# Kernel tuning notes

Hardware: AMD Instinct MI355X
Metric: run time of the kernel (lower is better)

## Reference

```python
import jax, jax.numpy as jnp
from jax import lax
import numpy as np

P = 2          # cost exponent: C(x,y) = |x-y|^p / p
BLUR = 0.05    # final epsilon = BLUR**P
SCALING = 0.5  # geomloss epsilon-scaling factor


def _cost(x, y):
    # squared Euclidean distance / 2  (geomloss p=2 cost), shape [N, M]
    sq = jnp.sum(x * x, axis=1)[:, None] + jnp.sum(y * y, axis=1)[None, :] - 2.0 * (x @ y.T)
    return jnp.maximum(sq, 0.0) * 0.5


def _softmin(eps, C, h):
    # h: log-weights (+ potential/eps) over columns of C; returns [rows]
    return -eps * jax.nn.logsumexp(h[None, :] - C / eps, axis=1)


def setup_inputs() -> dict:
    key = jax.random.key(0)
    k1, k2 = jax.random.split(key)
    N, M, D = 8192, 8192, 64
    g = jax.random.normal(k1, (N, D), jnp.float32)
    Y = jax.random.normal(k2, (M, D), jnp.float32) + 1.0  # shifted target measure
    # geomloss epsilon_schedule: diameter**p annealed by SCALING**p down to BLUR**p
    xy = np.concatenate([np.asarray(g), np.asarray(Y)], axis=0)
    diameter = float(np.linalg.norm(xy.max(0) - xy.min(0)))
    eps_list = ([diameter ** P]
                + [float(np.exp(e)) for e in np.arange(P * np.log(diameter), P * np.log(BLUR), P * np.log(SCALING))]
                + [BLUR ** P])
    return {"g": g, "Y": Y, "eps_list": jnp.asarray(eps_list, jnp.float32)}


def reference(g, Y, eps_list):
    x, y = g, Y
    N, M = x.shape[0], y.shape[0]
    a_log = jnp.full((N,), -jnp.log(jnp.float32(N)), x.dtype)  # uniform log-weights
    b_log = jnp.full((M,), -jnp.log(jnp.float32(M)), y.dtype)

    C_xy, C_yx = _cost(x, y), _cost(y, x)
    C_xx, C_yy = _cost(x, x), _cost(y, y)
    # Sinkhorn loop runs on detached costs (geomloss runs it under no_grad)
    sg = lax.stop_gradient
    Cxy_s, Cyx_s, Cxx_s, Cyy_s = sg(C_xy), sg(C_yx), sg(C_xx), sg(C_yy)

    eps0 = eps_list[0]
    f_aa = _softmin(eps0, Cxx_s, a_log)
    g_bb = _softmin(eps0, Cyy_s, b_log)
    g_ab = _softmin(eps0, Cyx_s, a_log)
    f_ba = _softmin(eps0, Cxy_s, b_log)

    def step(carry, eps):
        f_aa, g_bb, g_ab, f_ba = carry
        ft = _softmin(eps, Cxy_s, b_log + g_ab / eps)
        gt = _softmin(eps, Cyx_s, a_log + f_ba / eps)
        ftaa = _softmin(eps, Cxx_s, a_log + f_aa / eps)
        gtbb = _softmin(eps, Cyy_s, b_log + g_bb / eps)
        # symmetrized (averaged) dual updates, as in geomloss
        return (0.5 * (f_aa + ftaa), 0.5 * (g_bb + gtbb),
                0.5 * (g_ab + gt), 0.5 * (f_ba + ft)), None

    (f_aa, g_bb, g_ab, f_ba), _ = lax.scan(step, (f_aa, g_bb, g_ab, f_ba), eps_list)

    # last extrapolation at eps = blur**p: differentiable costs, detached potentials
    eps = eps_list[-1]
    f_ba_f = _softmin(eps, C_xy, sg(b_log + g_ab / eps))
    g_ab_f = _softmin(eps, C_yx, sg(a_log + f_ba / eps))
    f_aa_f = _softmin(eps, C_xx, sg(a_log + f_aa / eps))
    g_bb_f = _softmin(eps, C_yy, sg(b_log + g_bb / eps))

    # S_eps(alpha, beta) = <alpha, f_ba - f_aa> + <beta, g_ab - g_bb> (uniform weights)
    return jnp.mean(f_ba_f - f_aa_f) + jnp.mean(g_ab_f - g_bb_f)
```

## Files before the change

kernel.cpp:

```cpp
#include <hip/hip_runtime.h>
#include <math.h>

#define D 64
#define BR 128
#define NCHUNK 8
#define YLD 72
#define LOG2E 1.4426950408889634f
#define LN2   0.6931471805599453f

typedef __attribute__((ext_vector_type(8))) __bf16 bf16x8;
typedef __attribute__((ext_vector_type(4))) float  floatx4;
typedef __attribute__((ext_vector_type(2))) float  floatx2;

static __device__ __forceinline__ float exp2fast(float x) {
#if __has_builtin(__builtin_amdgcn_exp2f)
    return __builtin_amdgcn_exp2f(x);
#else
    return exp2f(x);
#endif
}
static __device__ __forceinline__ float log2fast(float x) {
#if __has_builtin(__builtin_amdgcn_logf)
    return __builtin_amdgcn_logf(x);
#else
    return log2f(x);
#endif
}
static __device__ __forceinline__ float max3f(float a, float b, float c) {
    return fmaxf(fmaxf(a, b), c);
}

static __device__ __forceinline__ unsigned short f2bf_rne(float f) {
    unsigned u = __float_as_uint(f);
    return (unsigned short)((u + 0x7fffu + ((u >> 16) & 1u)) >> 16);
}

struct OpDesc {
    const unsigned short* xh;
    const unsigned short* yh;
    const float* cc;
    const float* sqn_col;
    float* pm; float* ps;
    int n_rows, n_cols, symmetric, pad;
};
struct P4 { OpDesc op[4]; };

struct MDesc {
    const float* pm; const float* ps;
    const float* sqn_row;
    const float* oldpot;
    float* newpot;
    float* ccout;
    float wlog_c;
    int n_rows, mix, pad;
};
struct M4 { MDesc op[4]; };

__global__ void cvt_kernel(const float* __restrict__ x,
                           unsigned short* __restrict__ xh, int n_elem8)
{
    int i = blockIdx.x * blockDim.x + threadIdx.x;
    if (i >= n_elem8) return;
    const float4* xp = (const float4*)x;
    float4 v0 = xp[i * 2], v1 = xp[i * 2 + 1];
    float v[8] = {v0.x, v0.y, v0.z, v0.w, v1.x, v1.y, v1.z, v1.w};
    unsigned h[8];
#pragma unroll
    for (int k = 0; k < 8; ++k) h[k] = f2bf_rne(v[k]);
    uint4 ph;
    ph.x = h[0] | (h[1] << 16); ph.y = h[2] | (h[3] << 16);
    ph.z = h[4] | (h[5] << 16); ph.w = h[6] | (h[7] << 16);
    ((uint4*)xh)[i] = ph;
}

__global__ void sqnorm_kernel(const float* __restrict__ x, float* __restrict__ sqn, int n)
{
    int i = blockIdx.x * blockDim.x + threadIdx.x;
    if (i >= n) return;
    const float4* xp = (const float4*)(x + (size_t)i * D);
    float sum = 0.0f;
#pragma unroll
    for (int k = 0; k < D / 4; ++k) {
        float4 v = xp[k];
        sum += v.x * v.x + v.y * v.y + v.z * v.z + v.w * v.w;
    }
    sqn[i] = 0.5f * sum;
}

__global__ void init_cc_kernel(const float* __restrict__ sqn_x, const float* __restrict__ sqn_y,
                               float* cc0, float* cc1, float* cc2, float* cc3,
                               const float* __restrict__ eps_list,
                               float a_log, float b_log, int N, int M)
{
    int i = blockIdx.x * blockDim.x + threadIdx.x;
    float inv_e0 = 1.0f / eps_list[0];
    if (i < M) { float v = (b_log - sqn_y[i] * inv_e0) * LOG2E; cc0[i] = v; cc3[i] = v; }
    if (i < N) { float v = (a_log - sqn_x[i] * inv_e0) * LOG2E; cc1[i] = v; cc2[i] = v; }
}

__global__ __launch_bounds__(256)
void softmin_mfma4(P4 p4, const float* __restrict__ eps_list, int eps_idx)
{
    __shared__ __bf16 yth[128 * YLD];

    const OpDesc o = p4.op[blockIdx.z];
    const int t    = threadIdx.x;
    const int lane = t & 63;
    const int w    = t >> 6;
    const int lx   = lane & 15;
    const int q    = lane >> 4;
    const int row0 = blockIdx.x * BR;
    const int chunk = blockIdx.y;
    const int cols_per_chunk = o.n_cols / NCHUNK;
    const int nsub = cols_per_chunk / 128;

    const float eps     = eps_list[eps_idx];
    const float inv_eps = 1.0f / eps;
    const float scale2  = inv_eps * LOG2E;
    const floatx2 s2v   = (floatx2){scale2, scale2};
    const floatx4 Z4    = (floatx4){0.f, 0.f, 0.f, 0.f};

    bf16x8 ah[2][2];
    {
        const int r0 = row0 + w * 32;
#pragma unroll
        for (int rt = 0; rt < 2; ++rt)
#pragma unroll
            for (int ks = 0; ks < 2; ++ks)
                ah[rt][ks] = *(const bf16x8*)(o.xh + (size_t)(r0 + rt * 16 + lx) * D + ks * 32 + q * 8);
    }

    const int diag_blk = o.symmetric && ((row0 / cols_per_chunk) == chunk);
    float sqr[8];
    if (diag_blk) {
#pragma unroll
        for (int idx = 0; idx < 8; ++idx) {
            int row = row0 + w * 32 + (idx >> 2) * 16 + q * 4 + (idx & 3);
            sqr[idx] = o.sqn_col[row];
        }
    }

    float m[8], s[8];
#pragma unroll
    for (int i = 0; i < 8; ++i) { m[i] = -__builtin_inff(); s[i] = 0.0f; }

    for (int sub = 0; sub < nsub; ++sub) {
        const int col0 = chunk * cols_per_chunk + sub * 128;

        __syncthreads();
        {
            const uint4* gh = (const uint4*)(o.yh + (size_t)col0 * D);
#pragma unroll
            for (int i = 0; i < 4; ++i) {
                int c = t + i * 256;
                int row = c >> 3, part = c & 7;
                uint4 vh = gh[c];
                *(uint4*)(&yth[row * YLD + part * 8]) = vh;
            }
        }
        __syncthreads();

        float cc[8];
#pragma unroll
        for (int ct = 0; ct < 8; ++ct) cc[ct] = o.cc[col0 + ct * 16 + lx];

        floatx4 acc[8][2];
#pragma unroll
        for (int ct = 0; ct < 8; ++ct) {
            const int cl = ct * 16 + lx;
            bf16x8 bh0 = *(const bf16x8*)&yth[cl * YLD + q * 8];
            bf16x8 bh1 = *(const bf16x8*)&yth[cl * YLD + 32 + q * 8];
#pragma unroll
            for (int rt = 0; rt < 2; ++rt) {
                floatx4 a = __builtin_amdgcn_mfma_f32_16x16x32_bf16(ah[rt][0], bh0, Z4, 0, 0, 0);
                acc[ct][rt] = __builtin_amdgcn_mfma_f32_16x16x32_bf16(ah[rt][1], bh1, a, 0, 0, 0);
            }
        }

        if (diag_blk && col0 == row0) {
#pragma unroll
            for (int rt = 0; rt < 2; ++rt)
#pragma unroll
                for (int r = 0; r < 4; ++r) {
                    if (lx == q * 4 + r) {
                        const float v = 2.0f * sqr[rt * 4 + r];
#pragma unroll
                        for (int ct = 0; ct < 8; ++ct)
                            if (ct == w * 2 + rt) acc[ct][rt][r] = v;
                    }
                }
        }

        floatx2 ccv[4];
#pragma unroll
        for (int cp = 0; cp < 4; ++cp)
            ccv[cp] = (floatx2){cc[cp * 2], cc[cp * 2 + 1]};

#pragma unroll
        for (int rt = 0; rt < 2; ++rt)
#pragma unroll
            for (int r = 0; r < 4; ++r) {
                const int idx = rt * 4 + r;
                floatx2 zv[4];
#pragma unroll
                for (int cp = 0; cp < 4; ++cp) {
                    floatx2 av = (floatx2){acc[cp * 2][rt][r], acc[cp * 2 + 1][rt][r]};
                    zv[cp] = __builtin_elementwise_fma(av, s2v, ccv[cp]);
                }
                float M = max3f(zv[0].x, zv[0].y, zv[1].x);
                M = max3f(M, zv[1].y, zv[2].x);
                M = max3f(M, zv[2].y, zv[3].x);
                M = max3f(M, zv[3].y, m[idx]);
                const floatx2 Mv = (floatx2){M, M};
                floatx2 sv = (floatx2){0.f, 0.f};
#pragma unroll
                for (int cp = 0; cp < 4; ++cp) {
                    floatx2 dd = zv[cp] - Mv;
                    sv += (floatx2){exp2fast(dd.x), exp2fast(dd.y)};
                }
                s[idx] = fmaf(s[idx], exp2fast(m[idx] - M), sv.x + sv.y);
                m[idx] = M;
            }
    }

#pragma unroll
    for (int idx = 0; idx < 8; ++idx) {
        float mm = m[idx], ss = s[idx];
#pragma unroll
        for (int d = 1; d < 16; d <<= 1) {
            float mo = __shfl_xor(mm, d, 64);
            float so = __shfl_xor(ss, d, 64);
            float M = fmaxf(mm, mo);
            ss = ss * exp2fast(mm - M) + so * exp2fast(mo - M);
            mm = M;
        }
        if (lx == 0) {
            const int rt = idx >> 2, r = idx & 3;
            const int row = row0 + w * 32 + rt * 16 + q * 4 + r;
            o.pm[chunk * o.n_rows + row] = mm;
            o.ps[chunk * o.n_rows + row] = ss;
        }
    }
}

__global__ void softmin_merge4(M4 m4, const float* __restrict__ eps_list,
                               int eps_idx, int eps_idx_next)
{
    const MDesc o = m4.op[blockIdx.y];
    int i = blockIdx.x * blockDim.x + threadIdx.x;
    if (i >= o.n_rows) return;
    const float eps = eps_list[eps_idx];
    float M = -__builtin_inff();
    for (int c = 0; c < NCHUNK; ++c) M = fmaxf(M, o.pm[c * o.n_rows + i]);
    float S = 0.0f;
    for (int c = 0; c < NCHUNK; ++c) S += o.ps[c * o.n_rows + i] * exp2fast(o.pm[c * o.n_rows + i] - M);
    const float sq = o.sqn_row[i];
    float val = sq - eps * LN2 * (M + log2fast(S));
    float nv = o.mix ? 0.5f * (o.oldpot[i] + val) : val;
    o.newpot[i] = nv;
    if (o.ccout) {
        float inv_en = 1.0f / eps_list[eps_idx_next];
        o.ccout[i] = (o.wlog_c + (nv - sq) * inv_en) * LOG2E;
    }
}

__global__ void final_reduce(const float* __restrict__ f_ba_f, const float* __restrict__ f_aa_f,
                             const float* __restrict__ g_ab_f, const float* __restrict__ g_bb_f,
                             int n, int mcount, float* __restrict__ out)
{
    __shared__ float red[256];
    float s1 = 0.0f, s2 = 0.0f;
    for (int i = threadIdx.x; i < n; i += 256)      s1 += (f_ba_f[i] - f_aa_f[i]);
    for (int i = threadIdx.x; i < mcount; i += 256) s2 += (g_ab_f[i] - g_bb_f[i]);
    red[threadIdx.x] = s1 / (float)n + s2 / (float)mcount;
    __syncthreads();
    for (int off = 128; off > 0; off >>= 1) {
        if (threadIdx.x < off) red[threadIdx.x] += red[threadIdx.x + off];
        __syncthreads();
    }
    if (threadIdx.x == 0) out[0] = red[0];
}

extern "C" void kernel_launch(void* const* d_in, const int* in_sizes, int n_in,
                              void* d_out, int out_size, void* d_ws, size_t ws_size,
                              hipStream_t stream)
{
    const float* g        = (const float*)d_in[0];
    const float* Y        = (const float*)d_in[1];
    const float* eps_list = (const float*)d_in[2];
    const int N = in_sizes[0] / D;
    const int M = in_sizes[1] / D;
    const int L = in_sizes[2];
    const float a_log = -logf((float)N);
    const float b_log = -logf((float)M);
    const int NM = (N > M) ? N : M;
    const size_t PMS = (size_t)NCHUNK * NM;

    unsigned short* us = (unsigned short*)d_ws;
    unsigned short* gxh = us; us += (size_t)N * D;
    unsigned short* gyh = us; us += (size_t)M * D;

    float* ws = (float*)us;
    float* sqn_x = ws; ws += N;
    float* sqn_y = ws; ws += M;
    float* fba[2]; fba[0] = ws; ws += N; fba[1] = ws; ws += N;
    float* gab[2]; gab[0] = ws; ws += M; gab[1] = ws; ws += M;
    float* fa[2];  fa[0]  = ws; ws += N; fa[1]  = ws; ws += N;
    float* gb[2];  gb[0]  = ws; ws += M; gb[1]  = ws; ws += M;
    float* f_ba_f = ws; ws += N;
    float* g_ab_f = ws; ws += M;
    float* f_aa_f = ws; ws += N;
    float* g_bb_f = ws; ws += M;
    float* cc[2][4];
    for (int pbuf = 0; pbuf < 2; ++pbuf)
        for (int i = 0; i < 4; ++i) { cc[pbuf][i] = ws; ws += NM; }
    float* pm = ws; ws += 4 * PMS;
    float* psb = ws; ws += 4 * PMS;

    sqnorm_kernel<<<(N + 255) / 256, 256, 0, stream>>>(g, sqn_x, N);
    sqnorm_kernel<<<(M + 255) / 256, 256, 0, stream>>>(Y, sqn_y, M);
    cvt_kernel<<<(N * D / 8 + 255) / 256, 256, 0, stream>>>(g, gxh, N * D / 8);
    cvt_kernel<<<(M * D / 8 + 255) / 256, 256, 0, stream>>>(Y, gyh, M * D / 8);
    init_cc_kernel<<<(NM + 255) / 256, 256, 0, stream>>>(sqn_x, sqn_y,
        cc[0][0], cc[0][1], cc[0][2], cc[0][3], eps_list, a_log, b_log, N, M);

    auto phase = [&](int eidx, int eidx_next, int mix, int cur, int ccp, int writecc,
                     float* out0, float* out1, float* out2, float* out3) {
        P4 p;
        p.op[0] = { gxh, gyh, cc[ccp][0], sqn_y, pm + 0 * PMS, psb + 0 * PMS, N, M, 0, 0 };
        p.op[1] = { gyh, gxh, cc[ccp][1], sqn_x, pm + 1 * PMS, psb + 1 * PMS, M, N, 0, 0 };
        p.op[2] = { gxh, gxh, cc[ccp][2], sqn_x, pm + 2 * PMS, psb + 2 * PMS, N, N, 1, 0 };
        p.op[3] = { gyh, gyh, cc[ccp][3], sqn_y, pm + 3 * PMS, psb + 3 * PMS, M, M, 1, 0 };
        softmin_mfma4<<<dim3(NM / BR, NCHUNK, 4), 256, 0, stream>>>(p, eps_list, eidx);

        M4 mm;
        mm.op[0] = { pm + 0 * PMS, psb + 0 * PMS, sqn_x, fba[cur], out0,
                     writecc ? cc[ccp ^ 1][1] : nullptr, a_log, N, mix, 0 };
        mm.op[1] = { pm + 1 * PMS, psb + 1 * PMS, sqn_y, gab[cur], out1,
                     writecc ? cc[ccp ^ 1][0] : nullptr, b_log, M, mix, 0 };
        mm.op[2] = { pm + 2 * PMS, psb + 2 * PMS, sqn_x, fa[cur], out2,
                     writecc ? cc[ccp ^ 1][2] : nullptr, a_log, N, mix, 0 };
        mm.op[3] = { pm + 3 * PMS, psb + 3 * PMS, sqn_y, gb[cur], out3,
                     writecc ? cc[ccp ^ 1][3] : nullptr, b_log, M, mix, 0 };
        softmin_merge4<<<dim3((NM + 255) / 256, 4), 256, 0, stream>>>(mm, eps_list, eidx, eidx_next);
    };

    phase(0, 0, 0, 0, 0, 1, fba[0], gab[0], fa[0], gb[0]);
    int cur = 0, ccp = 1;

    for (int k = 0; k < L; ++k) {
        int en = (k + 1 < L) ? (k + 1) : (L - 1);
        phase(k, en, 1, cur, ccp, 1, fba[cur ^ 1], gab[cur ^ 1], fa[cur ^ 1], gb[cur ^ 1]);
        cur ^= 1; ccp ^= 1;
    }

    phase(L - 1, L - 1, 0, cur, ccp, 0, f_ba_f, g_ab_f, f_aa_f, g_bb_f);

    final_reduce<<<1, 256, 0, stream>>>(f_ba_f, f_aa_f, g_ab_f, g_bb_f, N, M, (float*)d_out);
}
```

Before: 1.251 ms.

## Convert softmin kernel to persistent blocks with atomic work-queue scheduling

The softmin MFMA kernel now launches a fixed grid of 768 persistent blocks that pull (op, row-block, chunk) work units from a global atomic counter instead of using a 3D grid. The counter is reset by init_cc and by each merge kernel so the next phase starts fresh. This is meant to improve load balance and cut block launch and tail overhead across the 2048 work units. It adds an atomic plus two barriers per unit, and the A-fragment and state setup now runs inside the unit loop.

```diff
diff --git a/kernel.cpp b/kernel.cpp
--- a/kernel.cpp
+++ b/kernel.cpp
@@ -5,6 +5,7 @@
 #define BR 128
 #define NCHUNK 8
 #define YLD 72
+#define NPERS 768
 #define LOG2E 1.4426950408889634f
 #define LN2   0.6931471805599453f
 
@@ -90,29 +91,28 @@
 __global__ void init_cc_kernel(const float* __restrict__ sqn_x, const float* __restrict__ sqn_y,
                                float* cc0, float* cc1, float* cc2, float* cc3,
                                const float* __restrict__ eps_list,
-                               float a_log, float b_log, int N, int M)
+                               float a_log, float b_log, int N, int M,
+                               int* __restrict__ counter)
 {
     int i = blockIdx.x * blockDim.x + threadIdx.x;
+    if (i == 0) counter[0] = 0;
     float inv_e0 = 1.0f / eps_list[0];
     if (i < M) { float v = (b_log - sqn_y[i] * inv_e0) * LOG2E; cc0[i] = v; cc3[i] = v; }
     if (i < N) { float v = (a_log - sqn_x[i] * inv_e0) * LOG2E; cc1[i] = v; cc2[i] = v; }
 }
 
 __global__ __launch_bounds__(256)
-void softmin_mfma4(P4 p4, const float* __restrict__ eps_list, int eps_idx)
+void softmin_mfma4(P4 p4, const float* __restrict__ eps_list, int eps_idx,
+                   int* __restrict__ counter, int rbmax, int nunits)
 {
     __shared__ __bf16 yth[128 * YLD];
-
-    const OpDesc o = p4.op[blockIdx.z];
+    __shared__ int u_sh;
+
     const int t    = threadIdx.x;
     const int lane = t & 63;
     const int w    = t >> 6;
     const int lx   = lane & 15;
     const int q    = lane >> 4;
-    const int row0 = blockIdx.x * BR;
-    const int chunk = blockIdx.y;
-    const int cols_per_chunk = o.n_cols / NCHUNK;
-    const int nsub = cols_per_chunk / 128;
 
     const float eps     = eps_list[eps_idx];
     const float inv_eps = 1.0f / eps;
@@ -120,132 +120,152 @@
     const floatx2 s2v   = (floatx2){scale2, scale2};
     const floatx4 Z4    = (floatx4){0.f, 0.f, 0.f, 0.f};
 
-    bf16x8 ah[2][2];
-    {
-        const int r0 = row0 + w * 32;
-#pragma unroll
-        for (int rt = 0; rt < 2; ++rt)
-#pragma unroll
-            for (int ks = 0; ks < 2; ++ks)
-                ah[rt][ks] = *(const bf16x8*)(o.xh + (size_t)(r0 + rt * 16 + lx) * D + ks * 32 + q * 8);
-    }
-
-    const int diag_blk = o.symmetric && ((row0 / cols_per_chunk) == chunk);
-    float sqr[8];
-    if (diag_blk) {
-#pragma unroll
-        for (int idx = 0; idx < 8; ++idx) {
-            int row = row0 + w * 32 + (idx >> 2) * 16 + q * 4 + (idx & 3);
-            sqr[idx] = o.sqn_col[row];
+    for (;;) {
+        __syncthreads();
+        if (t == 0) u_sh = atomicAdd(counter, 1);
+        __syncthreads();
+        const int u = u_sh;
+        if (u >= nunits) break;
+
+        const int op    = u / (rbmax * NCHUNK);
+        const int rem   = u - op * (rbmax * NCHUNK);
+        const int rb    = rem >> 3;
+        const int chunk = rem & (NCHUNK - 1);
+        const OpDesc o  = p4.op[op];
+        const int row0  = rb * BR;
+        if (row0 >= o.n_rows) continue;
+        const int cols_per_chunk = o.n_cols / NCHUNK;
+        const int nsub = cols_per_chunk / 128;
+
+        bf16x8 ah[2][2];
+        {
+            const int r0 = row0 + w * 32;
+#pragma unroll
+            for (int rt = 0; rt < 2; ++rt)
+#pragma unroll
+                for (int ks = 0; ks < 2; ++ks)
+                    ah[rt][ks] = *(const bf16x8*)(o.xh + (size_t)(r0 + rt * 16 + lx) * D + ks * 32 + q * 8);
         }
-    }
-
-    float m[8], s[8];
-#pragma unroll
-    for (int i = 0; i < 8; ++i) { m[i] = -__builtin_inff(); s[i] = 0.0f; }
-
-    for (int sub = 0; sub < nsub; ++sub) {
-        const int col0 = chunk * cols_per_chunk + sub * 128;
-
-        __syncthreads();
-        {
-            const uint4* gh = (const uint4*)(o.yh + (size_t)col0 * D);
-#pragma unroll
-            for (int i = 0; i < 4; ++i) {
-                int c = t + i * 256;
-                int row = c >> 3, part = c & 7;
-                uint4 vh = gh[c];
-                *(uint4*)(&yth[row * YLD + part * 8]) = vh;
+
+        const int diag_blk = o.symmetric && ((row0 / cols_per_chunk) == chunk);
+        float sqr[8];
+        if (diag_blk) {
+#pragma unroll
+            for (int idx = 0; idx < 8; ++idx) {
+                int row = row0 + w * 32 + (idx >> 2) * 16 + q * 4 + (idx & 3);
+                sqr[idx] = o.sqn_col[row];
             }
         }
-        __syncthreads();
-
-        float cc[8];
-#pragma unroll
-        for (int ct = 0; ct < 8; ++ct) cc[ct] = o.cc[col0 + ct * 16 + lx];
-
-        floatx4 acc[8][2];
-#pragma unroll
-        for (int ct = 0; ct < 8; ++ct) {
-            const int cl = ct * 16 + lx;
-            bf16x8 bh0 = *(const bf16x8*)&yth[cl * YLD + q * 8];
-            bf16x8 bh1 = *(const bf16x8*)&yth[cl * YLD + 32 + q * 8];
-#pragma unroll
-            for (int rt = 0; rt < 2; ++rt) {
-                floatx4 a = __builtin_amdgcn_mfma_f32_16x16x32_bf16(ah[rt][0], bh0, Z4, 0, 0, 0);
-                acc[ct][rt] = __builtin_amdgcn_mfma_f32_16x16x32_bf16(ah[rt][1], bh1, a, 0, 0, 0);
-            }
-        }
-
-        if (diag_blk && col0 == row0) {
+
+        float m[8], s[8];
+#pragma unroll
+        for (int i = 0; i < 8; ++i) { m[i] = -__builtin_inff(); s[i] = 0.0f; }
+
+        for (int sub = 0; sub < nsub; ++sub) {
+            const int col0 = chunk * cols_per_chunk + sub * 128;
+
+            __syncthreads();
+            {
+                const uint4* gh = (const uint4*)(o.yh + (size_t)col0 * D);
+#pragma unroll
+                for (int i = 0; i < 4; ++i) {
+                    int c = t + i * 256;
+                    int row = c >> 3, part = c & 7;
+                    uint4 vh = gh[c];
+                    *(uint4*)(&yth[row * YLD + part * 8]) = vh;
+                }
+            }
+            __syncthreads();
+
+            float cc[8];
+#pragma unroll
+            for (int ct = 0; ct < 8; ++ct) cc[ct] = o.cc[col0 + ct * 16 + lx];
+
+            floatx4 acc[8][2];
+#pragma unroll
+            for (int ct = 0; ct < 8; ++ct) {
+                const int cl = ct * 16 + lx;
+                bf16x8 bh0 = *(const bf16x8*)&yth[cl * YLD + q * 8];
+                bf16x8 bh1 = *(const bf16x8*)&yth[cl * YLD + 32 + q * 8];
+#pragma unroll
+                for (int rt = 0; rt < 2; ++rt) {
+                    floatx4 a = __builtin_amdgcn_mfma_f32_16x16x32_bf16(ah[rt][0], bh0, Z4, 0, 0, 0);
+                    acc[ct][rt] = __builtin_amdgcn_mfma_f32_16x16x32_bf16(ah[rt][1], bh1, a, 0, 0, 0);
+                }
+            }
+
+            if (diag_blk && col0 == row0) {
+#pragma unroll
+                for (int rt = 0; rt < 2; ++rt)
+#pragma unroll
+                    for (int r = 0; r < 4; ++r) {
+                        if (lx == q * 4 + r) {
+                            const float v = 2.0f * sqr[rt * 4 + r];
+#pragma unroll
+                            for (int ct = 0; ct < 8; ++ct)
+                                if (ct == w * 2 + rt) acc[ct][rt][r] = v;
+                        }
+                    }
+            }
+
+            floatx2 ccv[4];
+#pragma unroll
+            for (int cp = 0; cp < 4; ++cp)
+                ccv[cp] = (floatx2){cc[cp * 2], cc[cp * 2 + 1]};
+
 #pragma unroll
             for (int rt = 0; rt < 2; ++rt)
 #pragma unroll
                 for (int r = 0; r < 4; ++r) {
-                    if (lx == q * 4 + r) {
-                        const float v = 2.0f * sqr[rt * 4 + r];
-#pragma unroll
-                        for (int ct = 0; ct < 8; ++ct)
-                            if (ct == w * 2 + rt) acc[ct][rt][r] = v;
+                    const int idx = rt * 4 + r;
+                    floatx2 zv[4];
+#pragma unroll
+                    for (int cp = 0; cp < 4; ++cp) {
+                        floatx2 av = (floatx2){acc[cp * 2][rt][r], acc[cp * 2 + 1][rt][r]};
+                        zv[cp] = __builtin_elementwise_fma(av, s2v, ccv[cp]);
                     }
+                    float M = max3f(zv[0].x, zv[0].y, zv[1].x);
+                    M = max3f(M, zv[1].y, zv[2].x);
+                    M = max3f(M, zv[2].y, zv[3].x);
+                    M = max3f(M, zv[3].y, m[idx]);
+                    const floatx2 Mv = (floatx2){M, M};
+                    floatx2 sv = (floatx2){0.f, 0.f};
+#pragma unroll
+                    for (int cp = 0; cp < 4; ++cp) {
+                        floatx2 dd = zv[cp] - Mv;
+                        sv += (floatx2){exp2fast(dd.x), exp2fast(dd.y)};
+                    }
+                    s[idx] = fmaf(s[idx], exp2fast(m[idx] - M), sv.x + sv.y);
+                    m[idx] = M;
                 }
         }
 
-        floatx2 ccv[4];
-#pragma unroll
-        for (int cp = 0; cp < 4; ++cp)
-            ccv[cp] = (floatx2){cc[cp * 2], cc[cp * 2 + 1]};
-
-#pragma unroll
-        for (int rt = 0; rt < 2; ++rt)
-#pragma unroll
-            for (int r = 0; r < 4; ++r) {
-                const int idx = rt * 4 + r;
-                floatx2 zv[4];
-#pragma unroll
-                for (int cp = 0; cp < 4; ++cp) {
-                    floatx2 av = (floatx2){acc[cp * 2][rt][r], acc[cp * 2 + 1][rt][r]};
-                    zv[cp] = __builtin_elementwise_fma(av, s2v, ccv[cp]);
-                }
-                float M = max3f(zv[0].x, zv[0].y, zv[1].x);
-                M = max3f(M, zv[1].y, zv[2].x);
-                M = max3f(M, zv[2].y, zv[3].x);
-                M = max3f(M, zv[3].y, m[idx]);
-                const floatx2 Mv = (floatx2){M, M};
-                floatx2 sv = (floatx2){0.f, 0.f};
-#pragma unroll
-                for (int cp = 0; cp < 4; ++cp) {
-                    floatx2 dd = zv[cp] - Mv;
-                    sv += (floatx2){exp2fast(dd.x), exp2fast(dd.y)};
-                }
-                s[idx] = fmaf(s[idx], exp2fast(m[idx] - M), sv.x + sv.y);
-                m[idx] = M;
-            }
-    }
-
-#pragma unroll
-    for (int idx = 0; idx < 8; ++idx) {
-        float mm = m[idx], ss = s[idx];
-#pragma unroll
-        for (int d = 1; d < 16; d <<= 1) {
-            float mo = __shfl_xor(mm, d, 64);
-            float so = __shfl_xor(ss, d, 64);
-            float M = fmaxf(mm, mo);
-            ss = ss * exp2fast(mm - M) + so * exp2fast(mo - M);
-            mm = M;
+#pragma unroll
+        for (int idx = 0; idx < 8; ++idx) {
+            float mm = m[idx], ss = s[idx];
+#pragma unroll
+            for (int d = 1; d < 16; d <<= 1) {
+                float mo = __shfl_xor(mm, d, 64);
+                float so = __shfl_xor(ss, d, 64);
+                float M = fmaxf(mm, mo);
+                ss = ss * exp2fast(mm - M) + so * exp2fast(mo - M);
+                mm = M;
+            }
+            if (lx == 0) {
+                const int rt = idx >> 2, r = idx & 3;
+                const int row = row0 + w * 32 + rt * 16 + q * 4 + r;
+                o.pm[chunk * o.n_rows + row] = mm;
+                o.ps[chunk * o.n_rows + row] = ss;
+            }
         }
-        if (lx == 0) {
-            const int rt = idx >> 2, r = idx & 3;
-            const int row = row0 + w * 32 + rt * 16 + q * 4 + r;
-            o.pm[chunk * o.n_rows + row] = mm;
-            o.ps[chunk * o.n_rows + row] = ss;
-        }
     }
 }
 
 __global__ void softmin_merge4(M4 m4, const float* __restrict__ eps_list,
-                               int eps_idx, int eps_idx_next)
-{
+                               int eps_idx, int eps_idx_next, int* __restrict__ counter)
+{
+    if (blockIdx.x == 0 && blockIdx.y == 0 && threadIdx.x == 0)
+        counter[0] = 0;
     const MDesc o = m4.op[blockIdx.y];
     int i = blockIdx.x * blockDim.x + threadIdx.x;
     if (i >= o.n_rows) return;
@@ -294,6 +314,8 @@
     const float a_log = -logf((float)N);
     const float b_log = -logf((float)M);
     const int NM = (N > M) ? N : M;
+    const int rbmax = NM / BR;
+    const int nunits = 4 * rbmax * NCHUNK;
     const size_t PMS = (size_t)NCHUNK * NM;
 
     unsigned short* us = (unsigned short*)d_ws;
@@ -316,13 +338,14 @@
         for (int i = 0; i < 4; ++i) { cc[pbuf][i] = ws; ws += NM; }
     float* pm = ws; ws += 4 * PMS;
     float* psb = ws; ws += 4 * PMS;
+    int* counter = (int*)ws;
 
     sqnorm_kernel<<<(N + 255) / 256, 256, 0, stream>>>(g, sqn_x, N);
     sqnorm_kernel<<<(M + 255) / 256, 256, 0, stream>>>(Y, sqn_y, M);
     cvt_kernel<<<(N * D / 8 + 255) / 256, 256, 0, stream>>>(g, gxh, N * D / 8);
     cvt_kernel<<<(M * D / 8 + 255) / 256, 256, 0, stream>>>(Y, gyh, M * D / 8);
     init_cc_kernel<<<(NM + 255) / 256, 256, 0, stream>>>(sqn_x, sqn_y,
-        cc[0][0], cc[0][1], cc[0][2], cc[0][3], eps_list, a_log, b_log, N, M);
+        cc[0][0], cc[0][1], cc[0][2], cc[0][3], eps_list, a_log, b_log, N, M, counter);
 
     auto phase = [&](int eidx, int eidx_next, int mix, int cur, int ccp, int writecc,
                      float* out0, float* out1, float* out2, float* out3) {
@@ -331,7 +354,7 @@
         p.op[1] = { gyh, gxh, cc[ccp][1], sqn_x, pm + 1 * PMS, psb + 1 * PMS, M, N, 0, 0 };
         p.op[2] = { gxh, gxh, cc[ccp][2], sqn_x, pm + 2 * PMS, psb + 2 * PMS, N, N, 1, 0 };
         p.op[3] = { gyh, gyh, cc[ccp][3], sqn_y, pm + 3 * PMS, psb + 3 * PMS, M, M, 1, 0 };
-        softmin_mfma4<<<dim3(NM / BR, NCHUNK, 4), 256, 0, stream>>>(p, eps_list, eidx);
+        softmin_mfma4<<<NPERS, 256, 0, stream>>>(p, eps_list, eidx, counter, rbmax, nunits);
 
         M4 mm;
         mm.op[0] = { pm + 0 * PMS, psb + 0 * PMS, sqn_x, fba[cur], out0,
@@ -342,7 +365,8 @@
                      writecc ? cc[ccp ^ 1][2] : nullptr, a_log, N, mix, 0 };
         mm.op[3] = { pm + 3 * PMS, psb + 3 * PMS, sqn_y, gb[cur], out3,
                      writecc ? cc[ccp ^ 1][3] : nullptr, b_log, M, mix, 0 };
-        softmin_merge4<<<dim3((NM + 255) / 256, 4), 256, 0, stream>>>(mm, eps_list, eidx, eidx_next);
+        softmin_merge4<<<dim3((NM + 255) / 256, 4), 256, 0, stream>>>(mm, eps_list, eidx,
+                                                                      eidx_next, counter);
     };
 
     phase(0, 0, 0, 0, 0, 1, fba[0], gab[0], fa[0], gb[0]);
```

After: 1.463 ms. +16.9%, slower.
